# Performance work log

Hardware: AMD Instinct MI355X
Metric: run time of the kernel (lower is better)

Reference implementation:

```python
import jax, jax.numpy as jnp
import numpy as np

N = 50000   # vertices
E = 25000   # hyperedges
NNZ = 400000  # incidence pairs (v, e)
D_IN = 512
D_OUT = 512  # heads * out_channels, heads=1


def setup_inputs() -> dict:
    key = jax.random.key(0)
    kx, kw, kv, ke = jax.random.split(key, 4)
    X = jax.random.normal(kx, (N, D_IN), dtype=jnp.float32)
    W = jax.random.normal(kw, (D_OUT, D_IN), dtype=jnp.float32) * 0.02  # nn.Linear weight [out,in]
    vidx = jax.random.randint(kv, (NNZ,), 0, N, dtype=jnp.int32)
    eidx = jax.random.randint(ke, (NNZ,), 0, E, dtype=jnp.int32)
    # degE = 1/|e| (hyperedge size), degV = 1/deg(v), as precomputed by hyperg
    ones = jnp.ones((NNZ,), dtype=jnp.float32)
    edge_sz = jax.ops.segment_sum(ones, eidx, num_segments=E)
    vert_dg = jax.ops.segment_sum(ones, vidx, num_segments=N)
    degE = 1.0 / jnp.maximum(edge_sz, 1.0)
    degV = 1.0 / jnp.maximum(vert_dg, 1.0)
    Wdiag = jnp.ones((E,), dtype=jnp.float32)
    return {"X": X, "W": W, "degE": degE, "degV": degV, "Wdiag": Wdiag,
            "vidx": vidx, "eidx": eidx}


def reference(X, W, degE, degV, Wdiag, vidx, eidx):
    # Dense projection: X @ W^T (nn.Linear, no bias)
    Xp = jnp.einsum('nd,od->no', X, W)                      # [N, D_OUT]
    # Stage 1: vertex -> hyperedge (first_aggr: mean via degE), weighted by Wdiag
    Xe = jax.ops.segment_sum(Xp[vidx], eidx, num_segments=E)  # [E, D_OUT]
    Xe = Xe * (degE * Wdiag)[:, None]
    # Stage 2: hyperedge -> vertex, normalized by degV
    Xv = jax.ops.segment_sum(Xe[eidx], vidx, num_segments=N)  # [N, D_OUT]
    Xv = Xv * degV[:, None]
    return Xv
```

## Files before the change

kernel.cpp:

```cpp
#include <hip/hip_runtime.h>

typedef unsigned short u16;
typedef unsigned int   u32;
typedef __attribute__((ext_vector_type(4))) float f32x4;
typedef __attribute__((ext_vector_type(4))) u32   u32x4;
typedef __attribute__((ext_vector_type(8))) __bf16 bf16x8;

constexpr int NV   = 50000;
constexpr int NE   = 25000;
constexpr int NNZp = 400000;
constexpr int D    = 512;
constexpr int MP   = 50048;
constexpr int NBE  = 25;
constexpr int NBV  = 49;
constexpr int SG1  = 391;
constexpr int SG2  = 1563;

static __device__ __forceinline__ u16 f2bf(float f) {
  u32 u = __float_as_uint(f);
  u32 r = (u + 0x7fffu + ((u >> 16) & 1u)) >> 16;
  return (u16)r;
}
static __device__ __forceinline__ u32 pk2(float a, float b) {
  return (u32)f2bf(a) | ((u32)f2bf(b) << 16);
}

static __device__ __forceinline__ void gload_lds16(const u16* g, u16* l) {
  __builtin_amdgcn_global_load_lds(
      (const __attribute__((address_space(1))) u32*)g,
      (__attribute__((address_space(3))) u32*)l, 16, 0, 0);
}

__global__ void zero_kernel(int* cntE, int* cntV) {
  int i = blockIdx.x * 256 + threadIdx.x;
  if (i < NE) cntE[i] = 0;
  if (i < NV) cntV[i] = 0;
}

__global__ void hist_kernel(const int* __restrict__ vidx, const int* __restrict__ eidx,
                            int* cntE, int* cntV) {
  int i = blockIdx.x * 256 + threadIdx.x;
  if (i < NNZp) {
    atomicAdd(&cntE[eidx[i]], 1);
    atomicAdd(&cntV[vidx[i]], 1);
  }
}

__global__ __launch_bounds__(256) void scan1_kernel(
    const int* __restrict__ cntE, const int* __restrict__ cntV,
    int* offE, int* offV, int* blkSum) {
  const bool isE = blockIdx.x < NBE;
  const int* cnt = isE ? cntE : cntV;
  int* off = isE ? offE : offV;
  const int len = isE ? NE : NV;
  const int t = threadIdx.x;
  const int base = (isE ? blockIdx.x : blockIdx.x - NBE) * 1024 + t * 4;
  int4 c = {0, 0, 0, 0};
  if (base + 4 <= len) c = *(const int4*)(cnt + base);
  else {
    if (base + 0 < len) c.x = cnt[base + 0];
    if (base + 1 < len) c.y = cnt[base + 1];
    if (base + 2 < len) c.z = cnt[base + 2];
    if (base + 3 < len) c.w = cnt[base + 3];
  }
  int s = c.x + c.y + c.z + c.w;
  __shared__ int sm[256];
  sm[t] = s;
  __syncthreads();
  for (int d = 1; d < 256; d <<= 1) {
    int u = (t >= d) ? sm[t - d] : 0;
    __syncthreads();
    sm[t] += u;
    __syncthreads();
  }
  int ex = sm[t] - s;
  int4 o;
  o.x = ex; o.y = o.x + c.x; o.z = o.y + c.y; o.w = o.z + c.z;
  if (base + 4 <= len) *(int4*)(off + base) = o;
  else {
    if (base + 0 < len) off[base + 0] = o.x;
    if (base + 1 < len) off[base + 1] = o.y;
    if (base + 2 < len) off[base + 2] = o.z;
    if (base + 3 < len) off[base + 3] = o.w;
  }
  if (t == 255) blkSum[blockIdx.x] = sm[255];
}

__global__ void scan2_kernel(int* blkSum) {
  int wv = threadIdx.x >> 6, lane = threadIdx.x & 63;
  int off = wv ? NBE : 0, len = wv ? NBV : NBE;
  int v = (lane < len) ? blkSum[off + lane] : 0;
  int incl = v;
#pragma unroll
  for (int d = 1; d < 64; d <<= 1) {
    int u = __shfl_up(incl, d, 64);
    if (lane >= d) incl += u;
  }
  if (lane < len) blkSum[off + lane] = incl - v;
}

__global__ __launch_bounds__(256) void scan3_kernel(
    int* offE, int* offV, int* curE, int* curV, const int* __restrict__ blkSum) {
  const bool isE = blockIdx.x < NBE;
  int* off = isE ? offE : offV;
  int* cur = isE ? curE : curV;
  const int len = isE ? NE : NV;
  const int pref = blkSum[blockIdx.x];
  const int base = (isE ? blockIdx.x : blockIdx.x - NBE) * 1024 + threadIdx.x * 4;
  if (base + 4 <= len) {
    int4 o = *(int4*)(off + base);
    o.x += pref; o.y += pref; o.z += pref; o.w += pref;
    *(int4*)(off + base) = o;
    *(int4*)(cur + base) = o;
  } else {
    for (int q = 0; q < 4; q++)
      if (base + q < len) { int v = off[base + q] + pref; off[base + q] = v; cur[base + q] = v; }
  }
}

__global__ void scatter_kernel(const int* __restrict__ vidx, const int* __restrict__ eidx,
                               int* curE, int* curV, int* csr_ev, int* csr_ve) {
  int i = blockIdx.x * 256 + threadIdx.x;
  if (i < NNZp) {
    int e = eidx[i], v = vidx[i];
    csr_ev[atomicAdd(&curE[e], 1)] = v;
    csr_ve[atomicAdd(&curV[v], 1)] = e;
  }
}

__global__ __launch_bounds__(256) void convert_kernel(
    const float* __restrict__ X, const float* __restrict__ W,
    u16* __restrict__ Xb, u16* __restrict__ Wb) {
  constexpr size_t NX = (size_t)NV * D;
  size_t i = ((size_t)blockIdx.x * 256 + threadIdx.x) * 8;
  const float* src;
  u16* dst;
  if (i < NX) { src = X + i; dst = Xb + i; }
  else        { src = W + (i - NX); dst = Wb + (i - NX); }
  f32x4 a = *(const f32x4*)src;
  f32x4 b = *(const f32x4*)(src + 4);
  u32x4 p = { pk2(a[0], a[1]), pk2(a[2], a[3]), pk2(b[0], b[1]), pk2(b[2], b[3]) };
  *(u32x4*)dst = p;
}

__global__ __launch_bounds__(256) void gemm_kernel(const u16* __restrict__ A,
                                                   const u16* __restrict__ B,
                                                   u16* __restrict__ C) {
  __shared__ u16 sA[128 * 32];
  __shared__ u16 sB[128 * 32];
  const int tid  = threadIdx.x;
  const int lane = tid & 63;
  const int wave = tid >> 6;
  const int bm = blockIdx.y * 128;
  const int bn = blockIdx.x * 128;
  const int wm = (wave >> 1) * 64;
  const int wn = (wave & 1) * 64;
  const int lr = lane & 15;
  const int lk = (lane >> 4) * 8;
  const int srow = lane >> 2;
  const int scol = (lane & 3) * 8;

  f32x4 acc[4][4] = {};

  for (int kt = 0; kt < D; kt += 32) {
    __syncthreads();
#pragma unroll
    for (int c = 0; c < 2; c++) {
      const int ar = wave * 16 + c * 64;
      gload_lds16(A + (size_t)(bm + ar + srow) * D + kt + scol, &sA[ar * 32]);
      gload_lds16(B + (size_t)(bn + ar + srow) * D + kt + scol, &sB[ar * 32]);
    }
    __syncthreads();

    bf16x8 af[4], bfr[4];
#pragma unroll
    for (int i = 0; i < 4; i++) af[i]  = *(const bf16x8*)&sA[(wm + i * 16 + lr) * 32 + lk];
#pragma unroll
    for (int j = 0; j < 4; j++) bfr[j] = *(const bf16x8*)&sB[(wn + j * 16 + lr) * 32 + lk];
#pragma unroll
    for (int i = 0; i < 4; i++)
#pragma unroll
      for (int j = 0; j < 4; j++)
        acc[i][j] = __builtin_amdgcn_mfma_f32_16x16x32_bf16(af[i], bfr[j], acc[i][j], 0, 0, 0);
  }

#pragma unroll
  for (int i = 0; i < 4; i++)
#pragma unroll
    for (int r = 0; r < 4; r++) {
      int row = bm + wm + i * 16 + (lane >> 4) * 4 + r;
      u16* crow = C + (size_t)row * D + bn + wn + lr;
#pragma unroll
      for (int j = 0; j < 4; j++) crow[j * 16] = f2bf(acc[i][j][r]);
    }
}

__global__ __launch_bounds__(256) void stage1_kernel(
    const u16* __restrict__ Xp, const int* __restrict__ offE, const int* __restrict__ cntE,
    const int* __restrict__ csr_ev, const float* __restrict__ degE,
    const float* __restrict__ Wdiag, u16* __restrict__ Xe) {
  const int wave = threadIdx.x >> 6;
  const int lane = threadIdx.x & 63;
  const int g    = lane >> 2;
  const int c    = lane & 3;
  const int bid  = blockIdx.x;
  const int xcd  = bid & 7;
  const int tmp  = bid >> 3;
  const int phase = (tmp >= SG1) ? 1 : 0;
  const int sg    = tmp - phase * SG1;
  const int slice = xcd + 8 * phase;
  const int e     = sg * 64 + wave * 16 + g;
  const int col0  = slice * 32 + c * 8;
  int start = 0, cnt = 0;
  if (e < NE) { start = offE[e]; cnt = cntE[e]; }
  float acc[8] = {};
  int nxt = (cnt > 0) ? csr_ev[start] : 0;
  for (int j = 0; j < cnt; j++) {
    int v = nxt;
    if (j + 1 < cnt) nxt = csr_ev[start + j + 1];
    u32x4 p = *(const u32x4*)(Xp + (size_t)v * D + col0);
#pragma unroll
    for (int q = 0; q < 4; q++) {
      u32 u = p[q];
      acc[2 * q]     += __uint_as_float(u << 16);
      acc[2 * q + 1] += __uint_as_float(u & 0xffff0000u);
    }
  }
  if (e < NE) {
    float s = degE[e] * Wdiag[e];
    u32x4 o = { pk2(acc[0] * s, acc[1] * s), pk2(acc[2] * s, acc[3] * s),
                pk2(acc[4] * s, acc[5] * s), pk2(acc[6] * s, acc[7] * s) };
    *(u32x4*)(Xe + (size_t)e * D + col0) = o;
  }
}

__global__ __launch_bounds__(256) void stage2_kernel(
    const u16* __restrict__ Xe, const int* __restrict__ offV, const int* __restrict__ cntV,
    const int* __restrict__ csr_ve, const float* __restrict__ degV, float* __restrict__ out) {
  const int wave = threadIdx.x >> 6;
  const int lane = threadIdx.x & 63;
  const int g    = lane >> 3;
  const int c    = lane & 7;
  const int slice = blockIdx.x & 7;
  const int sg    = blockIdx.x >> 3;
  const int v     = sg * 32 + wave * 8 + g;
  const int col0  = slice * 64 + c * 8;
  int start = 0, cnt = 0;
  if (v < NV) { start = offV[v]; cnt = cntV[v]; }
  float acc[8] = {};
  int nxt = (cnt > 0) ? csr_ve[start] : 0;
  for (int j = 0; j < cnt; j++) {
    int e = nxt;
    if (j + 1 < cnt) nxt = csr_ve[start + j + 1];
    u32x4 p = *(const u32x4*)(Xe + (size_t)e * D + col0);
#pragma unroll
    for (int q = 0; q < 4; q++) {
      u32 u = p[q];
      acc[2 * q]     += __uint_as_float(u << 16);
      acc[2 * q + 1] += __uint_as_float(u & 0xffff0000u);
    }
  }
  if (v < NV) {
    float s = degV[v];
    float* orow = out + (size_t)v * D + col0;
    f32x4 o0 = { acc[0] * s, acc[1] * s, acc[2] * s, acc[3] * s };
    f32x4 o1 = { acc[4] * s, acc[5] * s, acc[6] * s, acc[7] * s };
    *(f32x4*)orow = o0;
    *(f32x4*)(orow + 4) = o1;
  }
}

extern "C" void kernel_launch(void* const* d_in, const int* in_sizes, int n_in,
                              void* d_out, int out_size, void* d_ws, size_t ws_size,
                              hipStream_t stream) {
  const float* X     = (const float*)d_in[0];
  const float* W     = (const float*)d_in[1];
  const float* degE  = (const float*)d_in[2];
  const float* degV  = (const float*)d_in[3];
  const float* Wdiag = (const float*)d_in[4];
  const int*   vidx  = (const int*)d_in[5];
  const int*   eidx  = (const int*)d_in[6];
  float* out = (float*)d_out;

  char* p = (char*)d_ws;
  auto take = [&](size_t bytes) { char* r = p; p += (bytes + 255) & ~(size_t)255; return r; };
  u16* Xb     = (u16*)take((size_t)MP * D * 2);
  u16* Wb     = (u16*)take((size_t)D * D * 2);
  u16* Xp     = (u16*)take((size_t)MP * D * 2);
  u16* Xe     = (u16*)take((size_t)NE * D * 2);
  int* cntE   = (int*)take((size_t)NE * 4);
  int* offE   = (int*)take((size_t)NE * 4);
  int* curE   = (int*)take((size_t)NE * 4);
  int* cntV   = (int*)take((size_t)NV * 4);
  int* offV   = (int*)take((size_t)NV * 4);
  int* curV   = (int*)take((size_t)NV * 4);
  int* csr_ev = (int*)take((size_t)NNZp * 4);
  int* csr_ve = (int*)take((size_t)NNZp * 4);
  int* blkSum = (int*)take((size_t)(NBE + NBV) * 4);

  constexpr size_t NCONV = ((size_t)NV * D + (size_t)D * D) / 8 / 256;

  zero_kernel   <<<(NV + 255) / 256, 256, 0, stream>>>(cntE, cntV);
  hist_kernel   <<<(NNZp + 255) / 256, 256, 0, stream>>>(vidx, eidx, cntE, cntV);
  scan1_kernel  <<<NBE + NBV, 256, 0, stream>>>(cntE, cntV, offE, offV, blkSum);
  scan2_kernel  <<<1, 128, 0, stream>>>(blkSum);
  scan3_kernel  <<<NBE + NBV, 256, 0, stream>>>(offE, offV, curE, curV, blkSum);
  scatter_kernel<<<(NNZp + 255) / 256, 256, 0, stream>>>(vidx, eidx, curE, curV, csr_ev, csr_ve);
  convert_kernel<<<NCONV, 256, 0, stream>>>(X, W, Xb, Wb);
  gemm_kernel   <<<dim3(D / 128, MP / 128), 256, 0, stream>>>(Xb, Wb, Xp);
  stage1_kernel <<<SG1 * 16, 256, 0, stream>>>(Xp, offE, cntE, csr_ev, degE, Wdiag, Xe);
  stage2_kernel <<<SG2 * 8, 256, 0, stream>>>(Xe, offV, cntV, csr_ve, degV, out);
}
```

Before: 459.7 us.

## Aggregate raw features to hyperedges before projection, halving GEMM rows

Uses linearity to reorder the work: hyperedge sums are taken over the bf16 input X, and the GEMM then runs on 25k hyperedge rows instead of 50k vertex rows, with the degE·Wdiag scaling folded into the GEMM epilogue. Xb is stored column-tiled (32-wide slices) and the GEMM output is written in 64-wide slices, so each gather reads a compact contiguous region. The index loads are batched per lane group and broadcast with shuffles. The risks are that rows 25000 to 25087 of the GEMM input are never written by stage1 (their outputs are skipped), and that the bf16 rounding now happens at different points than before.

```diff
diff --git a/kernel.cpp b/kernel.cpp
--- a/kernel.cpp
+++ b/kernel.cpp
@@ -10,7 +10,7 @@
 constexpr int NE   = 25000;
 constexpr int NNZp = 400000;
 constexpr int D    = 512;
-constexpr int MP   = 50048;
+constexpr int MP2  = 25088;
 constexpr int NBE  = 25;
 constexpr int NBV  = 49;
 constexpr int SG1  = 391;
@@ -135,16 +135,65 @@
   size_t i = ((size_t)blockIdx.x * 256 + threadIdx.x) * 8;
   const float* src;
   u16* dst;
-  if (i < NX) { src = X + i; dst = Xb + i; }
-  else        { src = W + (i - NX); dst = Wb + (i - NX); }
+  if (i < NX) {
+    int n = (int)(i >> 9);
+    int col = (int)(i & 511);
+    int t = col >> 5, w = col & 31;
+    src = X + i;
+    dst = Xb + (size_t)t * NV * 32 + (size_t)n * 32 + w;
+  } else {
+    src = W + (i - NX);
+    dst = Wb + (i - NX);
+  }
   f32x4 a = *(const f32x4*)src;
   f32x4 b = *(const f32x4*)(src + 4);
   u32x4 p = { pk2(a[0], a[1]), pk2(a[2], a[3]), pk2(b[0], b[1]), pk2(b[2], b[3]) };
   *(u32x4*)dst = p;
 }
 
+__global__ __launch_bounds__(256) void stage1_kernel(
+    const u16* __restrict__ Xb, const int* __restrict__ offE, const int* __restrict__ cntE,
+    const int* __restrict__ csr_ev, u16* __restrict__ XeR) {
+  const int wave = threadIdx.x >> 6;
+  const int lane = threadIdx.x & 63;
+  const int g    = lane >> 2;
+  const int c    = lane & 3;
+  const int bid  = blockIdx.x;
+  const int xcd  = bid & 7;
+  const int tmp  = bid >> 3;
+  const int phase = (tmp >= SG1) ? 1 : 0;
+  const int sg    = tmp - phase * SG1;
+  const int t     = xcd + 8 * phase;
+  const int e     = sg * 64 + wave * 16 + g;
+  const u16* base = Xb + (size_t)t * NV * 32;
+  int start = 0, cnt = 0;
+  if (e < NE) { start = offE[e]; cnt = cntE[e]; }
+  float acc[8] = {};
+  for (int j0 = 0; j0 < cnt; j0 += 4) {
+    int idx = (j0 + c < cnt) ? csr_ev[start + j0 + c] : 0;
+    int kmax = min(4, cnt - j0);
+    for (int k = 0; k < kmax; k++) {
+      int v = __shfl(idx, (lane & ~3) | k, 64);
+      u32x4 p = *(const u32x4*)(base + (size_t)v * 32 + c * 8);
+#pragma unroll
+      for (int q = 0; q < 4; q++) {
+        u32 u = p[q];
+        acc[2 * q]     += __uint_as_float(u << 16);
+        acc[2 * q + 1] += __uint_as_float(u & 0xffff0000u);
+      }
+    }
+  }
+  if (e < NE) {
+    u32x4 o = { pk2(acc[0], acc[1]), pk2(acc[2], acc[3]),
+                pk2(acc[4], acc[5]), pk2(acc[6], acc[7]) };
+    *(u32x4*)(XeR + (size_t)e * D + t * 32 + c * 8) = o;
+  }
+}
+
 __global__ __launch_bounds__(256) void gemm_kernel(const u16* __restrict__ A,
                                                    const u16* __restrict__ B,
+                                                   const float* __restrict__ degE,
+                                                   const float* __restrict__ Wdiag,
                                                    u16* __restrict__ C) {
   __shared__ u16 sA[128 * 32];
   __shared__ u16 sB[128 * 32];
@@ -189,82 +238,51 @@
 #pragma unroll
     for (int r = 0; r < 4; r++) {
       int row = bm + wm + i * 16 + (lane >> 4) * 4 + r;
-      u16* crow = C + (size_t)row * D + bn + wn + lr;
-#pragma unroll
-      for (int j = 0; j < 4; j++) crow[j * 16] = f2bf(acc[i][j][r]);
+      if (row < NE) {
+        float se = degE[row] * Wdiag[row];
+#pragma unroll
+        for (int j = 0; j < 4; j++) {
+          int col = bn + wn + lr + j * 16;
+          int s = col >> 6, w = col & 63;
+          C[(size_t)s * MP2 * 64 + (size_t)row * 64 + w] = f2bf(acc[i][j][r] * se);
+        }
+      }
     }
 }
 
-__global__ __launch_bounds__(256) void stage1_kernel(
-    const u16* __restrict__ Xp, const int* __restrict__ offE, const int* __restrict__ cntE,
-    const int* __restrict__ csr_ev, const float* __restrict__ degE,
-    const float* __restrict__ Wdiag, u16* __restrict__ Xe) {
-  const int wave = threadIdx.x >> 6;
-  const int lane = threadIdx.x & 63;
-  const int g    = lane >> 2;
-  const int c    = lane & 3;
-  const int bid  = blockIdx.x;
-  const int xcd  = bid & 7;
-  const int tmp  = bid >> 3;
-  const int phase = (tmp >= SG1) ? 1 : 0;
-  const int sg    = tmp - phase * SG1;
-  const int slice = xcd + 8 * phase;
-  const int e     = sg * 64 + wave * 16 + g;
-  const int col0  = slice * 32 + c * 8;
-  int start = 0, cnt = 0;
-  if (e < NE) { start = offE[e]; cnt = cntE[e]; }
-  float acc[8] = {};
-  int nxt = (cnt > 0) ? csr_ev[start] : 0;
-  for (int j = 0; j < cnt; j++) {
-    int v = nxt;
-    if (j + 1 < cnt) nxt = csr_ev[start + j + 1];
-    u32x4 p = *(const u32x4*)(Xp + (size_t)v * D + col0);
-#pragma unroll
-    for (int q = 0; q < 4; q++) {
-      u32 u = p[q];
-      acc[2 * q]     += __uint_as_float(u << 16);
-      acc[2 * q + 1] += __uint_as_float(u & 0xffff0000u);
-    }
-  }
-  if (e < NE) {
-    float s = degE[e] * Wdiag[e];
-    u32x4 o = { pk2(acc[0] * s, acc[1] * s), pk2(acc[2] * s, acc[3] * s),
-                pk2(acc[4] * s, acc[5] * s), pk2(acc[6] * s, acc[7] * s) };
-    *(u32x4*)(Xe + (size_t)e * D + col0) = o;
-  }
-}
-
 __global__ __launch_bounds__(256) void stage2_kernel(
-    const u16* __restrict__ Xe, const int* __restrict__ offV, const int* __restrict__ cntV,
+    const u16* __restrict__ Xe2, const int* __restrict__ offV, const int* __restrict__ cntV,
     const int* __restrict__ csr_ve, const float* __restrict__ degV, float* __restrict__ out) {
   const int wave = threadIdx.x >> 6;
   const int lane = threadIdx.x & 63;
   const int g    = lane >> 3;
   const int c    = lane & 7;
-  const int slice = blockIdx.x & 7;
-  const int sg    = blockIdx.x >> 3;
-  const int v     = sg * 32 + wave * 8 + g;
-  const int col0  = slice * 64 + c * 8;
+  const int s    = blockIdx.x & 7;
+  const int sg   = blockIdx.x >> 3;
+  const int v    = sg * 32 + wave * 8 + g;
+  const u16* base = Xe2 + (size_t)s * MP2 * 64;
   int start = 0, cnt = 0;
   if (v < NV) { start = offV[v]; cnt = cntV[v]; }
   float acc[8] = {};
-  int nxt = (cnt > 0) ? csr_ve[start] : 0;
-  for (int j = 0; j < cnt; j++) {
-    int e = nxt;
-    if (j + 1 < cnt) nxt = csr_ve[start + j + 1];
-    u32x4 p = *(const u32x4*)(Xe + (size_t)e * D + col0);
-#pragma unroll
-    for (int q = 0; q < 4; q++) {
-      u32 u = p[q];
-      acc[2 * q]     += __uint_as_float(u << 16);
-      acc[2 * q + 1] += __uint_as_float(u & 0xffff0000u);
+  for (int j0 = 0; j0 < cnt; j0 += 8) {
+    int idx = (j0 + c < cnt) ? csr_ve[start + j0 + c] : 0;
+    int kmax = min(8, cnt - j0);
+    for (int k = 0; k < kmax; k++) {
+      int e = __shfl(idx, (lane & ~7) | k, 64);
+      u32x4 p = *(const u32x4*)(base + (size_t)e * 64 + c * 8);
+#pragma unroll
+      for (int q = 0; q < 4; q++) {
+        u32 u = p[q];
+        acc[2 * q]     += __uint_as_float(u << 16);
+        acc[2 * q + 1] += __uint_as_float(u & 0xffff0000u);
+      }
     }
   }
   if (v < NV) {
-    float s = degV[v];
-    float* orow = out + (size_t)v * D + col0;
-    f32x4 o0 = { acc[0] * s, acc[1] * s, acc[2] * s, acc[3] * s };
-    f32x4 o1 = { acc[4] * s, acc[5] * s, acc[6] * s, acc[7] * s };
+    float sc = degV[v];
+    float* orow = out + (size_t)v * D + s * 64 + c * 8;
+    f32x4 o0 = { acc[0] * sc, acc[1] * sc, acc[2] * sc, acc[3] * sc };
+    f32x4 o1 = { acc[4] * sc, acc[5] * sc, acc[6] * sc, acc[7] * sc };
     *(f32x4*)orow = o0;
     *(f32x4*)(orow + 4) = o1;
   }
@@ -284,10 +302,10 @@
 
   char* p = (char*)d_ws;
   auto take = [&](size_t bytes) { char* r = p; p += (bytes + 255) & ~(size_t)255; return r; };
-  u16* Xb     = (u16*)take((size_t)MP * D * 2);
+  u16* Xb     = (u16*)take((size_t)NV * D * 2);
   u16* Wb     = (u16*)take((size_t)D * D * 2);
-  u16* Xp     = (u16*)take((size_t)MP * D * 2);
-  u16* Xe     = (u16*)take((size_t)NE * D * 2);
+  u16* XeR    = (u16*)take((size_t)MP2 * D * 2);
+  u16* Xe2    = (u16*)take((size_t)MP2 * D * 2);
   int* cntE   = (int*)take((size_t)NE * 4);
   int* offE   = (int*)take((size_t)NE * 4);
   int* curE   = (int*)take((size_t)NE * 4);
@@ -307,7 +325,7 @@
   scan3_kernel  <<<NBE + NBV, 256, 0, stream>>>(offE, offV, curE, curV, blkSum);
   scatter_kernel<<<(NNZp + 255) / 256, 256, 0, stream>>>(vidx, eidx, curE, curV, csr_ev, csr_ve);
   convert_kernel<<<NCONV, 256, 0, stream>>>(X, W, Xb, Wb);
-  gemm_kernel   <<<dim3(D / 128, MP / 128), 256, 0, stream>>>(Xb, Wb, Xp);
-  stage1_kernel <<<SG1 * 16, 256, 0, stream>>>(Xp, offE, cntE, csr_ev, degE, Wdiag, Xe);
-  stage2_kernel <<<SG2 * 8, 256, 0, stream>>>(Xe, offV, cntV, csr_ve, degV, out);
-}
+  stage1_kernel <<<SG1 * 16, 256, 0, stream>>>(Xb, offE, cntE, csr_ev, XeR);
+  gemm_kernel   <<<dim3(D / 128, MP2 / 128), 256, 0, stream>>>(XeR, Wb, degE, Wdiag, Xe2);
+  stage2_kernel <<<SG2 * 8, 256, 0, stream>>>(Xe2, offV, cntV, csr_ve, degV, out);
+}
```

After: 434.2 us. -5.5%, faster.
